# Kernel optimization log

Measured on AMD Instinct MI355X. Metric: run time of the kernel, lower is better.

Reference implementation:

```python
import jax, jax.numpy as jnp
import numpy as np

N_NODES = 50000
N_EDGES = 1600000
DIM = 512


def setup_inputs() -> dict:
    key = jax.random.key(0)
    k1, k2, k3, k4, k5 = jax.random.split(key, 5)
    x = jax.random.normal(k1, (N_NODES, DIM), dtype=jnp.float32)
    adj_rows = jax.random.randint(k2, (N_EDGES,), 0, N_NODES, dtype=jnp.int32)
    adj_cols = jax.random.randint(k3, (N_EDGES,), 0, N_NODES, dtype=jnp.int32)
    adj_vals = jax.random.uniform(k4, (N_EDGES,), dtype=jnp.float32)
    # fc1 weight [out_dim, in_dim], kaiming-normal-ish init
    weight = jax.random.normal(k5, (DIM, DIM), dtype=jnp.float32) * np.float32(np.sqrt(2.0 / DIM))
    scale = jnp.full((1,), 1.5, dtype=jnp.float32)
    return {"x": x, "adj_rows": adj_rows, "adj_cols": adj_cols,
            "adj_vals": adj_vals, "weight": weight, "scale": scale}


def reference(x, adj_rows, adj_cols, adj_vals, weight, scale):
    # dropout in eval mode -> identity
    N, D = x.shape
    # dense linear: y = x @ W^T
    y = jnp.einsum('nd,od->no', x, weight)
    # sparse adj @ y  (COO SpMM via gather + segment_sum)
    y = jax.ops.segment_sum(adj_vals[:, None] * y[adj_cols], adj_rows,
                            num_segments=N)
    # sp_norm: mean-center over nodes, scale by global RMS^{-1} * (1+scale) * sqrt(D)
    y_t = y - jnp.mean(y, axis=0, keepdims=True)
    y_norm = jnp.mean(jnp.sum(y_t * y_t, axis=1)) ** -0.5
    y = y_t * y_norm * (1.0 + scale) * jnp.float32(np.sqrt(D))
    # activation (relu), then residual (input_dim == output_dim)
    y = jax.nn.relu(y)
    return y + x
```

## Files before the change

### kernel.cpp

```cpp
#include <hip/hip_runtime.h>
#include <hip/hip_bf16.h>
#include <cstdint>
#include <cstddef>

#define N_NODES 50000
#define DIM 512
#define N_EDGES 1600000
#define NT 25
#define NB (N_NODES * NT)

typedef __bf16 bf16;
typedef __bf16 bf16x8 __attribute__((ext_vector_type(8)));
typedef __bf16 bf16x4 __attribute__((ext_vector_type(4)));
typedef float floatx4 __attribute__((ext_vector_type(4)));

__global__ void cast_kernel(const float* __restrict__ in, bf16* __restrict__ out, int n4) {
    int i = blockIdx.x * blockDim.x + threadIdx.x;
    if (i >= n4) return;
    float4 v = reinterpret_cast<const float4*>(in)[i];
    bf16x4 o;
    o[0] = (bf16)v.x; o[1] = (bf16)v.y; o[2] = (bf16)v.z; o[3] = (bf16)v.w;
    reinterpret_cast<bf16x4*>(out)[i] = o;
}

__global__ void hist_kernel(const int* __restrict__ rows, const int* __restrict__ cols,
                            int* __restrict__ cnt, int E) {
    int i = blockIdx.x * blockDim.x + threadIdx.x;
    if (i < E) {
        int key = rows[i] * NT + (cols[i] >> 11);
        atomicAdd(&cnt[key], 1);
    }
}

__global__ __launch_bounds__(1024) void scanA_kernel(const int* __restrict__ cnt,
                                                     int* __restrict__ row_start,
                                                     int* __restrict__ blksum, int n) {
    __shared__ int s[1024];
    const int t = threadIdx.x;
    int i = blockIdx.x * 1024 + t;
    int v = (i < n) ? cnt[i] : 0;
    s[t] = v;
    __syncthreads();
    for (int off = 1; off < 1024; off <<= 1) {
        int u = (t >= off) ? s[t - off] : 0;
        __syncthreads();
        s[t] += u;
        __syncthreads();
    }
    if (i < n) row_start[i] = s[t] - v;
    if (t == 1023) blksum[blockIdx.x] = s[1023];
}

__global__ __launch_bounds__(1024) void scanB_kernel(const int* __restrict__ blksum,
                                                     int* __restrict__ blkoff, int nb) {
    __shared__ int s[1024];
    const int t = threadIdx.x;
    const int base = t * 2;
    int a = (base < nb) ? blksum[base] : 0;
    int b = (base + 1 < nb) ? blksum[base + 1] : 0;
    s[t] = a + b;
    __syncthreads();
    for (int off = 1; off < 1024; off <<= 1) {
        int u = (t >= off) ? s[t - off] : 0;
        __syncthreads();
        s[t] += u;
        __syncthreads();
    }
    int excl = (t == 0) ? 0 : s[t - 1];
    if (base < nb) blkoff[base] = excl;
    if (base + 1 < nb) blkoff[base + 1] = excl + a;
}

__global__ __launch_bounds__(1024) void scanC_kernel(int* __restrict__ row_start,
                                                     const int* __restrict__ blkoff,
                                                     int* __restrict__ cursor, int n) {
    int i = blockIdx.x * 1024 + threadIdx.x;
    if (i >= n) return;
    int v = row_start[i] + blkoff[i >> 10];
    row_start[i] = v;
    cursor[i] = v;
    if (i == n - 1) row_start[n] = N_EDGES;
}

__global__ void scatter_kernel(const int* __restrict__ rows, const int* __restrict__ cols,
                               const float* __restrict__ vals, int* __restrict__ cursor,
                               int2* __restrict__ ecv, int E) {
    int i = blockIdx.x * blockDim.x + threadIdx.x;
    if (i >= E) return;
    int c = cols[i];
    int key = rows[i] * NT + (c >> 11);
    int p = atomicAdd(&cursor[key], 1);
    ecv[p] = make_int2(c, __float_as_int(vals[i]));
}

__global__ __launch_bounds__(256) void gemm_kernel(const bf16* __restrict__ A,
                                                   const bf16* __restrict__ B,
                                                   bf16* __restrict__ C) {
    __shared__ bf16 lA[128 * 32];
    __shared__ bf16 lB[128 * 32];
    const int t = threadIdx.x;
    const int wave = t >> 6;
    const int lane = t & 63;
    const int rowBase = blockIdx.x * 128;
    const int colBase = blockIdx.y * 128;
    const int wm = (wave >> 1) * 64;
    const int wn = (wave & 1) * 64;
    floatx4 acc[4][4] = {};

    const int r_a = t >> 2;
    const int kk = (t & 3) * 8;

    const int l15 = lane & 15;
    const int koff = (lane >> 4) * 8;

    for (int k0 = 0; k0 < DIM; k0 += 32) {
#pragma unroll
        for (int j = 0; j < 2; j++) {
            int row = rowBase + r_a + j * 64;
            if (row > N_NODES - 1) row = N_NODES - 1;
            const bf16* g = A + (size_t)row * DIM + k0 + kk;
            bf16* l = lA + wave * 512 + j * 2048;
            __builtin_amdgcn_global_load_lds(
                (const __attribute__((address_space(1))) void*)g,
                (__attribute__((address_space(3))) void*)l, 16, 0, 0);
        }
#pragma unroll
        for (int j = 0; j < 2; j++) {
            int row = colBase + r_a + j * 64;
            const bf16* g = B + (size_t)row * DIM + k0 + kk;
            bf16* l = lB + wave * 512 + j * 2048;
            __builtin_amdgcn_global_load_lds(
                (const __attribute__((address_space(1))) void*)g,
                (__attribute__((address_space(3))) void*)l, 16, 0, 0);
        }
        __syncthreads();
        bf16x8 af[4], bfr[4];
#pragma unroll
        for (int i = 0; i < 4; i++)
            af[i] = *reinterpret_cast<const bf16x8*>(lA + (wm + i * 16 + l15) * 32 + koff);
#pragma unroll
        for (int j = 0; j < 4; j++)
            bfr[j] = *reinterpret_cast<const bf16x8*>(lB + (wn + j * 16 + l15) * 32 + koff);
#pragma unroll
        for (int i = 0; i < 4; i++)
#pragma unroll
            for (int j = 0; j < 4; j++)
                acc[i][j] = __builtin_amdgcn_mfma_f32_16x16x32_bf16(af[i], bfr[j], acc[i][j], 0, 0, 0);
        __syncthreads();
    }
    const int rquad = (lane >> 4) * 4;
#pragma unroll
    for (int i = 0; i < 4; i++) {
#pragma unroll
        for (int reg = 0; reg < 4; reg++) {
            int gr = rowBase + wm + i * 16 + rquad + reg;
            if (gr >= N_NODES) continue;
#pragma unroll
            for (int j = 0; j < 4; j++) {
                int gc = colBase + wn + j * 16 + l15;
                C[(size_t)gr * DIM + gc] = (bf16)acc[i][j][reg];
            }
        }
    }
}

__device__ __forceinline__ float blo(uint32_t w) { return __uint_as_float(w << 16); }
__device__ __forceinline__ float bhi(uint32_t w) { return __uint_as_float(w & 0xffff0000u); }

__device__ __forceinline__ void fmac8(float* acc, float v, const uint4& w) {
    acc[0] += v * blo(w.x); acc[1] += v * bhi(w.x);
    acc[2] += v * blo(w.y); acc[3] += v * bhi(w.y);
    acc[4] += v * blo(w.z); acc[5] += v * bhi(w.z);
    acc[6] += v * blo(w.w); acc[7] += v * bhi(w.w);
}

__global__ __launch_bounds__(256) void spmm_kernel(const int* __restrict__ row_start,
                                                   const int2* __restrict__ ecv,
                                                   const bf16* __restrict__ y,
                                                   float* __restrict__ y2) {
    const int wave = threadIdx.x >> 6;
    const int lane = threadIdx.x & 63;
    const int r = blockIdx.x * 4 + wave;
    const int s = row_start[r * NT];
    const int e = row_start[(r + 1) * NT];
    float acc[8] = {0.f, 0.f, 0.f, 0.f, 0.f, 0.f, 0.f, 0.f};
    const uint32_t* yb = reinterpret_cast<const uint32_t*>(y);

    int i = s;
    for (; i + 3 < e; i += 4) {
        int2 e0 = ecv[i], e1 = ecv[i + 1], e2 = ecv[i + 2], e3 = ecv[i + 3];
        uint4 w0 = *reinterpret_cast<const uint4*>(yb + (size_t)e0.x * 256 + lane * 4);
        uint4 w1 = *reinterpret_cast<const uint4*>(yb + (size_t)e1.x * 256 + lane * 4);
        uint4 w2 = *reinterpret_cast<const uint4*>(yb + (size_t)e2.x * 256 + lane * 4);
        uint4 w3 = *reinterpret_cast<const uint4*>(yb + (size_t)e3.x * 256 + lane * 4);
        fmac8(acc, __int_as_float(e0.y), w0);
        fmac8(acc, __int_as_float(e1.y), w1);
        fmac8(acc, __int_as_float(e2.y), w2);
        fmac8(acc, __int_as_float(e3.y), w3);
    }
    for (; i < e; i++) {
        int2 e0 = ecv[i];
        uint4 w0 = *reinterpret_cast<const uint4*>(yb + (size_t)e0.x * 256 + lane * 4);
        fmac8(acc, __int_as_float(e0.y), w0);
    }
    float4* out = reinterpret_cast<float4*>(y2 + (size_t)r * DIM + lane * 8);
    out[0] = make_float4(acc[0], acc[1], acc[2], acc[3]);
    out[1] = make_float4(acc[4], acc[5], acc[6], acc[7]);
}

__global__ __launch_bounds__(256) void reduce_kernel(const float* __restrict__ y2,
                                                     float* __restrict__ colsum,
                                                     float* __restrict__ totsq) {
    const int t = threadIdx.x;
    const int d2 = t * 2;
    float c0 = 0.f, c1 = 0.f, sq = 0.f;
    for (int r = blockIdx.x; r < N_NODES; r += gridDim.x) {
        float2 v = *reinterpret_cast<const float2*>(y2 + (size_t)r * DIM + d2);
        c0 += v.x; c1 += v.y;
        sq += v.x * v.x + v.y * v.y;
    }
    atomicAdd(&colsum[d2], c0);
    atomicAdd(&colsum[d2 + 1], c1);
    __shared__ float ssq[256];
    ssq[t] = sq;
    __syncthreads();
    for (int off = 128; off > 0; off >>= 1) {
        if (t < off) ssq[t] += ssq[t + off];
        __syncthreads();
    }
    if (t == 0) atomicAdd(totsq, ssq[0]);
}

__global__ void scalar_kernel(const float* __restrict__ colsum, const float* __restrict__ totsq,
                              const float* __restrict__ scale, float* __restrict__ sfac) {
    __shared__ float sm[512];
    const int t = threadIdx.x;
    float mu = colsum[t] * (1.0f / N_NODES);
    sm[t] = mu * mu;
    __syncthreads();
    for (int off = 256; off > 0; off >>= 1) {
        if (t < off) sm[t] += sm[t + off];
        __syncthreads();
    }
    if (t == 0) {
        float var = totsq[0] * (1.0f / N_NODES) - sm[0];
        sfac[0] = rsqrtf(var) * (1.0f + scale[0]) * sqrtf((float)DIM);
    }
}

__global__ void final_kernel(float* __restrict__ y2, const float* __restrict__ x,
                             const float* __restrict__ colsum, const float* __restrict__ sfac,
                             int n4) {
    int i = blockIdx.x * blockDim.x + threadIdx.x;
    if (i >= n4) return;
    const float invN = 1.0f / N_NODES;
    float4 v = reinterpret_cast<float4*>(y2)[i];
    float4 xv = reinterpret_cast<const float4*>(x)[i];
    float4 mu = reinterpret_cast<const float4*>(colsum)[i & 127];
    float s = sfac[0];
    v.x = fmaxf((v.x - mu.x * invN) * s, 0.0f) + xv.x;
    v.y = fmaxf((v.y - mu.y * invN) * s, 0.0f) + xv.y;
    v.z = fmaxf((v.z - mu.z * invN) * s, 0.0f) + xv.z;
    v.w = fmaxf((v.w - mu.w * invN) * s, 0.0f) + xv.w;
    reinterpret_cast<float4*>(y2)[i] = v;
}

extern "C" void kernel_launch(void* const* d_in, const int* in_sizes, int n_in,
                              void* d_out, int out_size, void* d_ws, size_t ws_size,
                              hipStream_t stream) {
    const float* x        = (const float*)d_in[0];
    const int*   adj_rows = (const int*)d_in[1];
    const int*   adj_cols = (const int*)d_in[2];
    const float* adj_vals = (const float*)d_in[3];
    const float* weight   = (const float*)d_in[4];
    const float* scale    = (const float*)d_in[5];
    float* out = (float*)d_out;

    char* ws = (char*)d_ws;
    size_t off = 0;
    auto alloc = [&](size_t b) {
        char* p = ws + off;
        off += (b + 255) & ~(size_t)255;
        return p;
    };
    const int nblk = (NB + 1023) / 1024;
    bf16*  xb        = (bf16*)alloc((size_t)N_NODES * DIM * 2);
    int2*  ecv       = (int2*)xb;
    bf16*  Wb        = (bf16*)alloc((size_t)DIM * DIM * 2);
    bf16*  y         = (bf16*)alloc((size_t)N_NODES * DIM * 2);
    int*   cnt       = (int*)alloc((size_t)NB * 4);
    int*   cursor    = cnt;
    int*   row_start = (int*)alloc((size_t)(NB + 1) * 4);
    int*   blksum    = (int*)alloc((size_t)nblk * 4);
    int*   blkoff    = (int*)alloc((size_t)nblk * 4);
    float* colsum    = (float*)alloc(512 * 4);
    float* totsq     = (float*)alloc(4);
    float* sfac      = (float*)alloc(4);
    (void)ws_size; (void)in_sizes; (void)n_in; (void)out_size;

    hipMemsetAsync(cnt, 0, (size_t)NB * 4, stream);
    hipMemsetAsync(colsum, 0, 512 * 4, stream);
    hipMemsetAsync(totsq, 0, 4, stream);

    const int n4x = N_NODES * DIM / 4;
    const int n4w = DIM * DIM / 4;
    cast_kernel<<<(n4x + 255) / 256, 256, 0, stream>>>(x, xb, n4x);
    cast_kernel<<<(n4w + 255) / 256, 256, 0, stream>>>(weight, Wb, n4w);

    gemm_kernel<<<dim3((N_NODES + 127) / 128, DIM / 128), 256, 0, stream>>>(xb, Wb, y);

    hist_kernel<<<(N_EDGES + 255) / 256, 256, 0, stream>>>(adj_rows, adj_cols, cnt, N_EDGES);
    scanA_kernel<<<nblk, 1024, 0, stream>>>(cnt, row_start, blksum, NB);
    scanB_kernel<<<1, 1024, 0, stream>>>(blksum, blkoff, nblk);
    scanC_kernel<<<nblk, 1024, 0, stream>>>(row_start, blkoff, cursor, NB);
    scatter_kernel<<<(N_EDGES + 255) / 256, 256, 0, stream>>>(adj_rows, adj_cols, adj_vals,
                                                              cursor, ecv, N_EDGES);

    spmm_kernel<<<N_NODES / 4, 256, 0, stream>>>(row_start, ecv, y, out);

    reduce_kernel<<<256, 256, 0, stream>>>(out, colsum, totsq);
    scalar_kernel<<<1, 512, 0, stream>>>(colsum, totsq, scale, sfac);
    final_kernel<<<(n4x + 255) / 256, 256, 0, stream>>>(out, x, colsum, sfac, n4x);
}
```

Before: 732.6 us.

## Fuse x cast into GEMM, drop column tiling in CSR, split SpMM into feature halves

```diff
diff --git a/kernel.cpp b/kernel.cpp
--- a/kernel.cpp
+++ b/kernel.cpp
@@ -6,13 +6,15 @@
 #define N_NODES 50000
 #define DIM 512
 #define N_EDGES 1600000
-#define NT 25
-#define NB (N_NODES * NT)
+#define NB N_NODES
 
 typedef __bf16 bf16;
 typedef __bf16 bf16x8 __attribute__((ext_vector_type(8)));
 typedef __bf16 bf16x4 __attribute__((ext_vector_type(4)));
 typedef float floatx4 __attribute__((ext_vector_type(4)));
+typedef float floatx2 __attribute__((ext_vector_type(2)));
+typedef unsigned int uintx2 __attribute__((ext_vector_type(2)));
+typedef unsigned int uintx4 __attribute__((ext_vector_type(4)));
 
 __global__ void cast_kernel(const float* __restrict__ in, bf16* __restrict__ out, int n4) {
     int i = blockIdx.x * blockDim.x + threadIdx.x;
@@ -23,13 +25,9 @@
     reinterpret_cast<bf16x4*>(out)[i] = o;
 }
 
-__global__ void hist_kernel(const int* __restrict__ rows, const int* __restrict__ cols,
-                            int* __restrict__ cnt, int E) {
+__global__ void hist_kernel(const int* __restrict__ rows, int* __restrict__ cnt, int E) {
     int i = blockIdx.x * blockDim.x + threadIdx.x;
-    if (i < E) {
-        int key = rows[i] * NT + (cols[i] >> 11);
-        atomicAdd(&cnt[key], 1);
-    }
+    if (i < E) atomicAdd(&cnt[rows[i]], 1);
 }
 
 __global__ __launch_bounds__(1024) void scanA_kernel(const int* __restrict__ cnt,
@@ -84,81 +82,78 @@
 
 __global__ void scatter_kernel(const int* __restrict__ rows, const int* __restrict__ cols,
                                const float* __restrict__ vals, int* __restrict__ cursor,
-                               int2* __restrict__ ecv, int E) {
+                               unsigned long long* __restrict__ ecv, int E) {
     int i = blockIdx.x * blockDim.x + threadIdx.x;
     if (i >= E) return;
-    int c = cols[i];
-    int key = rows[i] * NT + (c >> 11);
-    int p = atomicAdd(&cursor[key], 1);
-    ecv[p] = make_int2(c, __float_as_int(vals[i]));
-}
-
-__global__ __launch_bounds__(256) void gemm_kernel(const bf16* __restrict__ A,
+    int r = rows[i];
+    int p = atomicAdd(&cursor[r], 1);
+    unsigned long long packed =
+        (unsigned long long)(unsigned int)cols[i] |
+        ((unsigned long long)(unsigned int)__float_as_uint(vals[i]) << 32);
+    __builtin_nontemporal_store(packed, &ecv[p]);
+}
+
+__global__ __launch_bounds__(512) void gemm_kernel(const float* __restrict__ A,
                                                    const bf16* __restrict__ B,
                                                    bf16* __restrict__ C) {
-    __shared__ bf16 lA[128 * 32];
-    __shared__ bf16 lB[128 * 32];
+    __shared__ bf16 lB[512 * 32];
     const int t = threadIdx.x;
     const int wave = t >> 6;
     const int lane = t & 63;
     const int rowBase = blockIdx.x * 128;
-    const int colBase = blockIdx.y * 128;
-    const int wm = (wave >> 1) * 64;
-    const int wn = (wave & 1) * 64;
-    floatx4 acc[4][4] = {};
-
-    const int r_a = t >> 2;
-    const int kk = (t & 3) * 8;
-
+    const int wm = (wave >> 1) * 32;
+    const int wn = (wave & 1) * 256;
     const int l15 = lane & 15;
-    const int koff = (lane >> 4) * 8;
+    const int koct = (lane >> 4) * 8;
+
+    floatx4 acc[2][16] = {};
 
     for (int k0 = 0; k0 < DIM; k0 += 32) {
 #pragma unroll
-        for (int j = 0; j < 2; j++) {
-            int row = rowBase + r_a + j * 64;
-            if (row > N_NODES - 1) row = N_NODES - 1;
-            const bf16* g = A + (size_t)row * DIM + k0 + kk;
-            bf16* l = lA + wave * 512 + j * 2048;
+        for (int j = 0; j < 4; j++) {
+            int idx = j * 512 + t;
+            int n = idx >> 2;
+            int ko = (idx & 3) * 8;
+            const bf16* g = B + (size_t)n * DIM + k0 + ko;
+            bf16* l = lB + (size_t)j * 4096 + wave * 512;
             __builtin_amdgcn_global_load_lds(
                 (const __attribute__((address_space(1))) void*)g,
                 (__attribute__((address_space(3))) void*)l, 16, 0, 0);
         }
-#pragma unroll
-        for (int j = 0; j < 2; j++) {
-            int row = colBase + r_a + j * 64;
-            const bf16* g = B + (size_t)row * DIM + k0 + kk;
-            bf16* l = lB + wave * 512 + j * 2048;
-            __builtin_amdgcn_global_load_lds(
-                (const __attribute__((address_space(1))) void*)g,
-                (__attribute__((address_space(3))) void*)l, 16, 0, 0);
+        bf16x8 af[2];
+#pragma unroll
+        for (int i = 0; i < 2; i++) {
+            int row = rowBase + wm + i * 16 + l15;
+            if (row > N_NODES - 1) row = N_NODES - 1;
+            const float* ga = A + (size_t)row * DIM + k0 + koct;
+            float4 fa = *reinterpret_cast<const float4*>(ga);
+            float4 fb = *reinterpret_cast<const float4*>(ga + 4);
+            bf16x8 v;
+            v[0] = (bf16)fa.x; v[1] = (bf16)fa.y; v[2] = (bf16)fa.z; v[3] = (bf16)fa.w;
+            v[4] = (bf16)fb.x; v[5] = (bf16)fb.y; v[6] = (bf16)fb.z; v[7] = (bf16)fb.w;
+            af[i] = v;
         }
         __syncthreads();
-        bf16x8 af[4], bfr[4];
-#pragma unroll
-        for (int i = 0; i < 4; i++)
-            af[i] = *reinterpret_cast<const bf16x8*>(lA + (wm + i * 16 + l15) * 32 + koff);
-#pragma unroll
-        for (int j = 0; j < 4; j++)
-            bfr[j] = *reinterpret_cast<const bf16x8*>(lB + (wn + j * 16 + l15) * 32 + koff);
-#pragma unroll
-        for (int i = 0; i < 4; i++)
-#pragma unroll
-            for (int j = 0; j < 4; j++)
-                acc[i][j] = __builtin_amdgcn_mfma_f32_16x16x32_bf16(af[i], bfr[j], acc[i][j], 0, 0, 0);
+#pragma unroll
+        for (int nt = 0; nt < 16; nt++) {
+            const bf16* bp = lB + (size_t)(wn + nt * 16 + l15) * 32 + koct;
+            bf16x8 bf = *reinterpret_cast<const bf16x8*>(bp);
+            acc[0][nt] = __builtin_amdgcn_mfma_f32_16x16x32_bf16(af[0], bf, acc[0][nt], 0, 0, 0);
+            acc[1][nt] = __builtin_amdgcn_mfma_f32_16x16x32_bf16(af[1], bf, acc[1][nt], 0, 0, 0);
+        }
         __syncthreads();
     }
     const int rquad = (lane >> 4) * 4;
 #pragma unroll
-    for (int i = 0; i < 4; i++) {
+    for (int i = 0; i < 2; i++) {
 #pragma unroll
         for (int reg = 0; reg < 4; reg++) {
             int gr = rowBase + wm + i * 16 + rquad + reg;
             if (gr >= N_NODES) continue;
 #pragma unroll
-            for (int j = 0; j < 4; j++) {
-                int gc = colBase + wn + j * 16 + l15;
-                C[(size_t)gr * DIM + gc] = (bf16)acc[i][j][reg];
+            for (int nt = 0; nt < 16; nt++) {
+                int gc = wn + nt * 16 + l15;
+                C[(size_t)gr * DIM + gc] = (bf16)acc[i][nt][reg];
             }
         }
     }
@@ -167,45 +162,54 @@
 __device__ __forceinline__ float blo(uint32_t w) { return __uint_as_float(w << 16); }
 __device__ __forceinline__ float bhi(uint32_t w) { return __uint_as_float(w & 0xffff0000u); }
 
-__device__ __forceinline__ void fmac8(float* acc, float v, const uint4& w) {
-    acc[0] += v * blo(w.x); acc[1] += v * bhi(w.x);
-    acc[2] += v * blo(w.y); acc[3] += v * bhi(w.y);
-    acc[4] += v * blo(w.z); acc[5] += v * bhi(w.z);
-    acc[6] += v * blo(w.w); acc[7] += v * bhi(w.w);
+__device__ __forceinline__ void fmac4(float* acc, unsigned long long e, const uintx2& w) {
+    float v = __uint_as_float((uint32_t)(e >> 32));
+    acc[0] += v * blo(w[0]); acc[1] += v * bhi(w[0]);
+    acc[2] += v * blo(w[1]); acc[3] += v * bhi(w[1]);
 }
 
 __global__ __launch_bounds__(256) void spmm_kernel(const int* __restrict__ row_start,
-                                                   const int2* __restrict__ ecv,
+                                                   const unsigned long long* __restrict__ ecv,
                                                    const bf16* __restrict__ y,
-                                                   float* __restrict__ y2) {
+                                                   float* __restrict__ y2, int dimOff) {
     const int wave = threadIdx.x >> 6;
     const int lane = threadIdx.x & 63;
     const int r = blockIdx.x * 4 + wave;
-    const int s = row_start[r * NT];
-    const int e = row_start[(r + 1) * NT];
-    float acc[8] = {0.f, 0.f, 0.f, 0.f, 0.f, 0.f, 0.f, 0.f};
-    const uint32_t* yb = reinterpret_cast<const uint32_t*>(y);
+    const int s = row_start[r];
+    const int e = row_start[r + 1];
+    float acc[4] = {0.f, 0.f, 0.f, 0.f};
+    const uintx2* yb = reinterpret_cast<const uintx2*>(
+        reinterpret_cast<const char*>(y) + (size_t)dimOff * 2 + (size_t)lane * 8);
 
     int i = s;
-    for (; i + 3 < e; i += 4) {
-        int2 e0 = ecv[i], e1 = ecv[i + 1], e2 = ecv[i + 2], e3 = ecv[i + 3];
-        uint4 w0 = *reinterpret_cast<const uint4*>(yb + (size_t)e0.x * 256 + lane * 4);
-        uint4 w1 = *reinterpret_cast<const uint4*>(yb + (size_t)e1.x * 256 + lane * 4);
-        uint4 w2 = *reinterpret_cast<const uint4*>(yb + (size_t)e2.x * 256 + lane * 4);
-        uint4 w3 = *reinterpret_cast<const uint4*>(yb + (size_t)e3.x * 256 + lane * 4);
-        fmac8(acc, __int_as_float(e0.y), w0);
-        fmac8(acc, __int_as_float(e1.y), w1);
-        fmac8(acc, __int_as_float(e2.y), w2);
-        fmac8(acc, __int_as_float(e3.y), w3);
+    for (; i + 7 < e; i += 8) {
+        unsigned long long e0 = __builtin_nontemporal_load(&ecv[i]);
+        unsigned long long e1 = __builtin_nontemporal_load(&ecv[i + 1]);
+        unsigned long long e2 = __builtin_nontemporal_load(&ecv[i + 2]);
+        unsigned long long e3 = __builtin_nontemporal_load(&ecv[i + 3]);
+        unsigned long long e4 = __builtin_nontemporal_load(&ecv[i + 4]);
+        unsigned long long e5 = __builtin_nontemporal_load(&ecv[i + 5]);
+        unsigned long long e6 = __builtin_nontemporal_load(&ecv[i + 6]);
+        unsigned long long e7 = __builtin_nontemporal_load(&ecv[i + 7]);
+        uintx2 w0 = yb[(size_t)(uint32_t)e0 * 128];
+        uintx2 w1 = yb[(size_t)(uint32_t)e1 * 128];
+        uintx2 w2 = yb[(size_t)(uint32_t)e2 * 128];
+        uintx2 w3 = yb[(size_t)(uint32_t)e3 * 128];
+        uintx2 w4 = yb[(size_t)(uint32_t)e4 * 128];
+        uintx2 w5 = yb[(size_t)(uint32_t)e5 * 128];
+        uintx2 w6 = yb[(size_t)(uint32_t)e6 * 128];
+        uintx2 w7 = yb[(size_t)(uint32_t)e7 * 128];
+        fmac4(acc, e0, w0); fmac4(acc, e1, w1); fmac4(acc, e2, w2); fmac4(acc, e3, w3);
+        fmac4(acc, e4, w4); fmac4(acc, e5, w5); fmac4(acc, e6, w6); fmac4(acc, e7, w7);
     }
     for (; i < e; i++) {
-        int2 e0 = ecv[i];
-        uint4 w0 = *reinterpret_cast<const uint4*>(yb + (size_t)e0.x * 256 + lane * 4);
-        fmac8(acc, __int_as_float(e0.y), w0);
-    }
-    float4* out = reinterpret_cast<float4*>(y2 + (size_t)r * DIM + lane * 8);
-    out[0] = make_float4(acc[0], acc[1], acc[2], acc[3]);
-    out[1] = make_float4(acc[4], acc[5], acc[6], acc[7]);
+        unsigned long long e0 = __builtin_nontemporal_load(&ecv[i]);
+        uintx2 w0 = yb[(size_t)(uint32_t)e0 * 128];
+        fmac4(acc, e0, w0);
+    }
+    floatx4 o; o[0] = acc[0]; o[1] = acc[1]; o[2] = acc[2]; o[3] = acc[3];
+    floatx4* out = reinterpret_cast<floatx4*>(y2 + (size_t)r * DIM + dimOff + lane * 4);
+    __builtin_nontemporal_store(o, out);
 }
 
 __global__ __launch_bounds__(256) void reduce_kernel(const float* __restrict__ y2,
@@ -215,9 +219,10 @@
     const int d2 = t * 2;
     float c0 = 0.f, c1 = 0.f, sq = 0.f;
     for (int r = blockIdx.x; r < N_NODES; r += gridDim.x) {
-        float2 v = *reinterpret_cast<const float2*>(y2 + (size_t)r * DIM + d2);
-        c0 += v.x; c1 += v.y;
-        sq += v.x * v.x + v.y * v.y;
+        floatx2 v = __builtin_nontemporal_load(
+            reinterpret_cast<const floatx2*>(y2 + (size_t)r * DIM + d2));
+        c0 += v[0]; c1 += v[1];
+        sq += v[0] * v[0] + v[1] * v[1];
     }
     atomicAdd(&colsum[d2], c0);
     atomicAdd(&colsum[d2 + 1], c1);
@@ -254,15 +259,15 @@
     int i = blockIdx.x * blockDim.x + threadIdx.x;
     if (i >= n4) return;
     const float invN = 1.0f / N_NODES;
-    float4 v = reinterpret_cast<float4*>(y2)[i];
-    float4 xv = reinterpret_cast<const float4*>(x)[i];
+    floatx4 v = __builtin_nontemporal_load(reinterpret_cast<floatx4*>(y2) + i);
+    floatx4 xv = __builtin_nontemporal_load(reinterpret_cast<const floatx4*>(x) + i);
     float4 mu = reinterpret_cast<const float4*>(colsum)[i & 127];
     float s = sfac[0];
-    v.x = fmaxf((v.x - mu.x * invN) * s, 0.0f) + xv.x;
-    v.y = fmaxf((v.y - mu.y * invN) * s, 0.0f) + xv.y;
-    v.z = fmaxf((v.z - mu.z * invN) * s, 0.0f) + xv.z;
-    v.w = fmaxf((v.w - mu.w * invN) * s, 0.0f) + xv.w;
-    reinterpret_cast<float4*>(y2)[i] = v;
+    v[0] = fmaxf((v[0] - mu.x * invN) * s, 0.0f) + xv[0];
+    v[1] = fmaxf((v[1] - mu.y * invN) * s, 0.0f) + xv[1];
+    v[2] = fmaxf((v[2] - mu.z * invN) * s, 0.0f) + xv[2];
+    v[3] = fmaxf((v[3] - mu.w * invN) * s, 0.0f) + xv[3];
+    __builtin_nontemporal_store(v, reinterpret_cast<floatx4*>(y2) + i);
 }
 
 extern "C" void kernel_launch(void* const* d_in, const int* in_sizes, int n_in,
@@ -284,39 +289,38 @@
         return p;
     };
     const int nblk = (NB + 1023) / 1024;
-    bf16*  xb        = (bf16*)alloc((size_t)N_NODES * DIM * 2);
-    int2*  ecv       = (int2*)xb;
+    bf16*  y         = (bf16*)alloc((size_t)N_NODES * DIM * 2);
+    unsigned long long* ecv = (unsigned long long*)alloc((size_t)N_EDGES * 8);
     bf16*  Wb        = (bf16*)alloc((size_t)DIM * DIM * 2);
-    bf16*  y         = (bf16*)alloc((size_t)N_NODES * DIM * 2);
     int*   cnt       = (int*)alloc((size_t)NB * 4);
     int*   cursor    = cnt;
     int*   row_start = (int*)alloc((size_t)(NB + 1) * 4);
     int*   blksum    = (int*)alloc((size_t)nblk * 4);
     int*   blkoff    = (int*)alloc((size_t)nblk * 4);
-    float* colsum    = (float*)alloc(512 * 4);
-    float* totsq     = (float*)alloc(4);
-    float* sfac      = (float*)alloc(4);
+    float* stats     = (float*)alloc(514 * 4);
+    float* colsum    = stats;
+    float* totsq     = stats + 512;
+    float* sfac      = stats + 513;
     (void)ws_size; (void)in_sizes; (void)n_in; (void)out_size;
 
     hipMemsetAsync(cnt, 0, (size_t)NB * 4, stream);
-    hipMemsetAsync(colsum, 0, 512 * 4, stream);
-    hipMemsetAsync(totsq, 0, 4, stream);
+    hipMemsetAsync(stats, 0, 514 * 4, stream);
 
     const int n4x = N_NODES * DIM / 4;
     const int n4w = DIM * DIM / 4;
-    cast_kernel<<<(n4x + 255) / 256, 256, 0, stream>>>(x, xb, n4x);
     cast_kernel<<<(n4w + 255) / 256, 256, 0, stream>>>(weight, Wb, n4w);
 
-    gemm_kernel<<<dim3((N_NODES + 127) / 128, DIM / 128), 256, 0, stream>>>(xb, Wb, y);
-
-    hist_kernel<<<(N_EDGES + 255) / 256, 256, 0, stream>>>(adj_rows, adj_cols, cnt, N_EDGES);
+    hist_kernel<<<(N_EDGES + 255) / 256, 256, 0, stream>>>(adj_rows, cnt, N_EDGES);
     scanA_kernel<<<nblk, 1024, 0, stream>>>(cnt, row_start, blksum, NB);
     scanB_kernel<<<1, 1024, 0, stream>>>(blksum, blkoff, nblk);
     scanC_kernel<<<nblk, 1024, 0, stream>>>(row_start, blkoff, cursor, NB);
     scatter_kernel<<<(N_EDGES + 255) / 256, 256, 0, stream>>>(adj_rows, adj_cols, adj_vals,
                                                               cursor, ecv, N_EDGES);
 
-    spmm_kernel<<<N_NODES / 4, 256, 0, stream>>>(row_start, ecv, y, out);
+    gemm_kernel<<<(N_NODES + 127) / 128, 512, 0, stream>>>(x, Wb, y);
+
+    spmm_kernel<<<N_NODES / 4, 256, 0, stream>>>(row_start, ecv, y, out, 0);
+    spmm_kernel<<<N_NODES / 4, 256, 0, stream>>>(row_start, ecv, y, out, 256);
 
     reduce_kernel<<<256, 256, 0, stream>>>(out, colsum, totsq);
     scalar_kernel<<<1, 512, 0, stream>>>(colsum, totsq, scale, sfac);
```

Measured after the change: 818.5 us. 1.12x slower.
